# Kernel tuning notes

Measured on AMD Instinct MI355X. Metric: run time of the kernel, lower is better.

Reference implementation:

```python
import jax, jax.numpy as jnp
import numpy as np

HEADS = 8
DIM_HEAD = 128
H = 32
W = 32
SCALE = DIM_HEAD ** (-0.5)


def rel_to_abs(x):
    # x: (b, nh, l, 2l-1) -> (b, nh, l, l) via pad/reshape trick
    b, nh, l, _ = x.shape
    x = jnp.pad(x, ((0, 0), (0, 0), (0, 0), (0, 1)))            # (b,nh,l,2l)
    flat = x.reshape(b, nh, l * 2 * l)
    flat = jnp.pad(flat, ((0, 0), (0, 0), (0, l - 1)))
    final = flat.reshape(b, nh, l + 1, 2 * l - 1)
    return final[:, :, :l, l - 1:]


def relative_logits_1d(q, rel_k):
    # q: (b,n,h,w,d), rel_k: (2w-1,d) -> (b,n,h,h,w,w)
    b, n, h, w, d = q.shape
    logits = jnp.einsum('bnhwd,rd->bnhwr', q, rel_k)
    logits = logits.reshape(b, n * h, w, 2 * w - 1)
    logits = rel_to_abs(logits).reshape(b, n, h, w, w)
    return jnp.broadcast_to(logits[:, :, :, None], (b, n, h, h, w, w))


def rel_pos_logits(q, rel_height, rel_width):
    # q: (b,n,h*w,d) -> (b,n,h*w,h*w)
    b, n, _, d = q.shape
    qh = q.reshape(b, n, H, W, d)
    # width logits: 'b n h H w W -> b n (h w) (H W)'
    rw = relative_logits_1d(qh, rel_width)                       # (b,n,h,H,w,W)
    rw = jnp.transpose(rw, (0, 1, 2, 4, 3, 5)).reshape(b, n, H * W, H * W)
    # height logits: q transposed to (b,n,w,h,d); result 'b n w W h H'
    qt = jnp.transpose(qh, (0, 1, 3, 2, 4))
    rh = relative_logits_1d(qt, rel_height)                      # (b,n,w,W,h,H)
    rh = jnp.transpose(rh, (0, 1, 4, 2, 5, 3)).reshape(b, n, H * W, H * W)
    return rw + rh


def setup_inputs() -> dict:
    key = jax.random.key(0)
    k1, k2, k3, k4 = jax.random.split(key, 4)
    featuremap = jax.random.normal(k1, (8, 512, H, W), dtype=jnp.float32)
    w_qkv = jax.random.normal(k2, (3 * HEADS * DIM_HEAD, 512), dtype=jnp.float32) * 0.02
    rel_height = jax.random.normal(k3, (2 * H - 1, DIM_HEAD), dtype=jnp.float32) * SCALE
    rel_width = jax.random.normal(k4, (2 * W - 1, DIM_HEAD), dtype=jnp.float32) * SCALE
    return {"featuremap": featuremap, "w_qkv": w_qkv,
            "rel_height": rel_height, "rel_width": rel_width}


def reference(featuremap, w_qkv, rel_height, rel_width):
    b, c, h, w = featuremap.shape
    n, d = HEADS, DIM_HEAD
    qkv = jnp.einsum('oc,bchw->bohw', w_qkv, featuremap)         # 1x1 conv, no bias
    q, k, v = jnp.split(qkv, 3, axis=1)

    def to_heads(t):  # 'b (n d) h w -> b n (h w) d'
        return jnp.transpose(t.reshape(b, n, d, h * w), (0, 1, 3, 2))

    q, k, v = to_heads(q), to_heads(k), to_heads(v)
    q = q * SCALE
    logits = jnp.einsum('bnxd,bnyd->bnxy', q, k)
    logits = logits + rel_pos_logits(q, rel_height, rel_width)
    weights = jax.nn.softmax(logits, axis=-1)
    attn_out = jnp.einsum('bnxy,bnyd->bnxd', weights, v)         # (b,n,hw,d)
    # 'b n (h w) d -> b (n d) h w'
    return jnp.transpose(attn_out, (0, 1, 3, 2)).reshape(b, n * d, h, w)
```

## Files before the change

### kernel.cpp

```cpp
#include <hip/hip_runtime.h>

#define BATCH 8
#define CIN   512
#define NH    8
#define DH    128
#define PP    1024
#define QK_SCALE 0.08838834764831845f

typedef unsigned int  u32;
typedef unsigned short u16;
typedef __attribute__((ext_vector_type(8)))  short short8;
typedef __attribute__((ext_vector_type(16))) float f32x16;
typedef __attribute__((ext_vector_type(4)))  u32 u32x4;

typedef __attribute__((address_space(1))) const u32 GU32;
typedef __attribute__((address_space(3))) u32 LU32;


__device__ inline u32 f2bf(float x) {
    u32 u = __float_as_uint(x);
    return (u + 0x7fffu + ((u >> 16) & 1u)) >> 16;
}
__device__ inline float bf2f(u32 h) { return __uint_as_float(h << 16); }

__device__ inline u32 cvtpk(float a, float b) {
    u32 r; asm("v_cvt_pk_bf16_f32 %0, %1, %2" : "=v"(r) : "v"(a), "v"(b)); return r;
}
__device__ inline void split2(float a, float b, u32& wh, u32& wl) {
    u32 h = cvtpk(a, b);
    float ha = __uint_as_float(h << 16);
    float hb = __uint_as_float(h & 0xffff0000u);
    wl = cvtpk(a - ha, b - hb);
    wh = h;
}

__device__ inline void cvt8(const float* v, float scl, uint4& hv, uint4& lv) {
    u32 h[8], l[8];
#pragma unroll
    for (int j = 0; j < 8; ++j) {
        float x = v[j] * scl;
        u32 hb = f2bf(x);
        float hf = bf2f(hb);
        u32 lb = f2bf(x - hf);
        h[j] = hb; l[j] = lb;
    }
    hv = make_uint4(h[0] | (h[1] << 16), h[2] | (h[3] << 16),
                    h[4] | (h[5] << 16), h[6] | (h[7] << 16));
    lv = make_uint4(l[0] | (l[1] << 16), l[2] | (l[3] << 16),
                    l[4] | (l[5] << 16), l[6] | (l[7] << 16));
}

__global__ __launch_bounds__(256) void wconv(
    const float* __restrict__ w, char* __restrict__ AIMG)
{
    const int gid = blockIdx.x * 256 + threadIdx.x;
    const int o  = gid >> 6;
    const int c0 = (gid & 63) << 3;
    const float scl = (o < 1024) ? QK_SCALE : 1.0f;
    float v[8];
    float4 v0 = *(const float4*)(w + (size_t)o * CIN + c0);
    float4 v1 = *(const float4*)(w + (size_t)o * CIN + c0 + 4);
    v[0]=v0.x; v[1]=v0.y; v[2]=v0.z; v[3]=v0.w;
    v[4]=v1.x; v[5]=v1.y; v[6]=v1.z; v[7]=v1.w;
    uint4 hv, lv; cvt8(v, scl, hv, lv);
    const int otile = o >> 7, row = o & 127, chunk = c0 >> 5, g = (c0 >> 3) & 3;
    char* base = AIMG + (size_t)(otile * 16 + chunk) * 16384
               + row * 64 + ((g ^ (row & 3)) << 4);
    *(uint4*)(base)        = hv;
    *(uint4*)(base + 8192) = lv;
}

__global__ __launch_bounds__(256) void fmconv(
    const float* __restrict__ fm, char* __restrict__ FIMG)
{
    __shared__ float Fs[32][128];
    const int t = threadIdx.x;
    const int chunk = blockIdx.x, ptile = blockIdx.y, b = blockIdx.z;
    const float* src = fm + ((size_t)(b * CIN + chunk * 32)) * PP + ptile * 128;
#pragma unroll
    for (int ii = 0; ii < 4; ++ii) {
        int idx = t + 256 * ii;
        int c = idx >> 5, p4 = idx & 31;
        *(float4*)(&Fs[c][p4 * 4]) = *(const float4*)(src + (size_t)c * PP + p4 * 4);
    }
    __syncthreads();
    const int p = t & 127, gb = (t >> 7) * 2;
#pragma unroll
    for (int gi = 0; gi < 2; ++gi) {
        const int g = gb + gi;
        float v[8];
#pragma unroll
        for (int j = 0; j < 8; ++j) v[j] = Fs[g * 8 + j][p];
        uint4 hv, lv; cvt8(v, 1.0f, hv, lv);
        char* base = FIMG + (size_t)((b * 8 + ptile) * 16 + chunk) * 16384
                   + p * 64 + ((g ^ (p & 3)) << 4);
        *(uint4*)(base)        = hv;
        *(uint4*)(base + 8192) = lv;
    }
}

__global__ __launch_bounds__(256) void relprep(
    const float* __restrict__ relH, const float* __restrict__ relW,
    char* __restrict__ RELIMG)
{
    const int idx = blockIdx.x * 256 + threadIdx.x;
    const int r = idx >> 4, g = idx & 15;
    float v[8];
    if (r < 63) {
        float4 v0 = *(const float4*)(relH + (size_t)r * DH + g * 8);
        float4 v1 = *(const float4*)(relH + (size_t)r * DH + g * 8 + 4);
        v[0]=v0.x; v[1]=v0.y; v[2]=v0.z; v[3]=v0.w;
        v[4]=v1.x; v[5]=v1.y; v[6]=v1.z; v[7]=v1.w;
    } else if (r < 126) {
        float4 v0 = *(const float4*)(relW + (size_t)(r - 63) * DH + g * 8);
        float4 v1 = *(const float4*)(relW + (size_t)(r - 63) * DH + g * 8 + 4);
        v[0]=v0.x; v[1]=v0.y; v[2]=v0.z; v[3]=v0.w;
        v[4]=v1.x; v[5]=v1.y; v[6]=v1.z; v[7]=v1.w;
    } else {
#pragma unroll
        for (int j = 0; j < 8; ++j) v[j] = 0.f;
    }
    uint4 hv, lv; cvt8(v, 1.0f, hv, lv);
    char* base = RELIMG + r * 256 + ((g ^ (r & 15)) << 4);
    *(uint4*)(base)         = hv;
    *(uint4*)(base + 32768) = lv;
}

__global__ __launch_bounds__(256, 2) void qkv_gemm(
    const char* __restrict__ AIMG, const char* __restrict__ FIMG,
    u16* __restrict__ Qhi, u16* __restrict__ Qlo,
    char* __restrict__ KIMG, char* __restrict__ VIMG)
{
    __shared__ char lds[65536];

    const int t = threadIdx.x, lane = t & 63, wid = t >> 6;
    const int l31 = lane & 31, h5 = lane >> 5;
    const int ptile = blockIdx.x, otile = blockIdx.y, b = blockIdx.z;
    const int wr = wid >> 1, wc = wid & 1;

    const char* Achunks = AIMG + (size_t)(otile * 16) * 16384;
    const char* Bchunks = FIMG + (size_t)((b * 8 + ptile) * 16) * 16384;

    const int half = wid & 1;
    const char* srcTile = (wid < 2) ? Achunks : Bchunks;
    char* dstBase0 = lds + ((wid < 2) ? 0 : 16384) + half * 8192;

    auto stageChunk = [&](int chunk, int par) {
        const char* src = srcTile + (size_t)chunk * 16384 + half * 8192 + lane * 16;
        char* dst = dstBase0 + par * 32768;
#pragma unroll
        for (int c = 0; c < 8; ++c)
            __builtin_amdgcn_global_load_lds((GU32*)(src + c * 1024),
                                             (LU32*)(dst + c * 1024), 16, 0, 0);
    };

    f32x16 acc[2][2];
#pragma unroll
    for (int i = 0; i < 2; ++i)
#pragma unroll
        for (int j = 0; j < 2; ++j)
#pragma unroll
            for (int r = 0; r < 16; ++r) acc[i][j][r] = 0.f;

    auto computeChunk = [&](int par) {
        const char* Abuf = lds + par * 32768;
        const char* Bbuf = Abuf + 16384;
#pragma unroll
        for (int ks = 0; ks < 2; ++ks) {
            short8 a_h[2], a_l[2], b_h[2], b_l[2];
#pragma unroll
            for (int ot = 0; ot < 2; ++ot) {
                const int row = wr * 64 + ot * 32 + l31;
                const int off = row * 64 + (((ks * 2 + h5) ^ (row & 3)) << 4);
                a_h[ot] = *(const short8*)(Abuf + off);
                a_l[ot] = *(const short8*)(Abuf + 8192 + off);
            }
#pragma unroll
            for (int pt = 0; pt < 2; ++pt) {
                const int col = wc * 64 + pt * 32 + l31;
                const int off = col * 64 + (((ks * 2 + h5) ^ (col & 3)) << 4);
                b_h[pt] = *(const short8*)(Bbuf + off);
                b_l[pt] = *(const short8*)(Bbuf + 8192 + off);
            }
#pragma unroll
            for (int ot = 0; ot < 2; ++ot)
#pragma unroll
                for (int pt = 0; pt < 2; ++pt) {
                    acc[ot][pt] = __builtin_amdgcn_mfma_f32_32x32x16_bf16(a_h[ot], b_h[pt], acc[ot][pt], 0, 0, 0);
                    acc[ot][pt] = __builtin_amdgcn_mfma_f32_32x32x16_bf16(a_h[ot], b_l[pt], acc[ot][pt], 0, 0, 0);
                    acc[ot][pt] = __builtin_amdgcn_mfma_f32_32x32x16_bf16(a_l[ot], b_h[pt], acc[ot][pt], 0, 0, 0);
                }
        }
    };

    stageChunk(0, 0);
    for (int ch = 0; ch < 15; ++ch) {
        stageChunk(ch + 1, (ch + 1) & 1);
        asm volatile("s_waitcnt vmcnt(8)" ::: "memory");
        __builtin_amdgcn_sched_barrier(0);
        __builtin_amdgcn_s_barrier();
        __builtin_amdgcn_sched_barrier(0);
        computeChunk(ch & 1);
        __builtin_amdgcn_s_barrier();
        __builtin_amdgcn_sched_barrier(0);
    }
    asm volatile("s_waitcnt vmcnt(0)" ::: "memory");
    __builtin_amdgcn_sched_barrier(0);
    __builtin_amdgcn_s_barrier();
    __builtin_amdgcn_sched_barrier(0);
    computeChunk(1);
    __syncthreads();

    float* Cs = (float*)lds;
#pragma unroll
    for (int ot = 0; ot < 2; ++ot)
#pragma unroll
        for (int pt = 0; pt < 2; ++pt)
#pragma unroll
            for (int r = 0; r < 16; ++r) {
                const int o = wr * 64 + ot * 32 + (r & 3) + 8 * (r >> 2) + 4 * h5;
                const int p = wc * 64 + pt * 32 + l31;
                Cs[o * 128 + (p ^ (o & 31))] = acc[ot][pt][r];
            }
    __syncthreads();

    const int tsel = otile >> 3;
    const int n    = otile & 7;
    const int bn   = b * NH + n;

    if (tsel == 0) {
        const int d0 = (t & 15) * 8, prow = t >> 4;
#pragma unroll
        for (int i = 0; i < 8; ++i) {
            const int p = prow + 16 * i;
            float v[8];
#pragma unroll
            for (int j = 0; j < 8; ++j)
                v[j] = Cs[(d0 + j) * 128 + (p ^ ((d0 + j) & 31))];
            uint4 hv, lv; cvt8(v, 1.0f, hv, lv);
            const size_t off = ((size_t)bn * PP + ptile * 128 + p) * DH + d0;
            *(uint4*)(Qhi + off) = hv;
            *(uint4*)(Qlo + off) = lv;
        }
    } else if (tsel == 1) {
        const int d0 = (t & 15) * 8, prow = t >> 4;
#pragma unroll
        for (int i = 0; i < 8; ++i) {
            const int p = prow + 16 * i;
            float v[8];
#pragma unroll
            for (int j = 0; j < 8; ++j)
                v[j] = Cs[(d0 + j) * 128 + (p ^ ((d0 + j) & 31))];
            uint4 hv, lv; cvt8(v, 1.0f, hv, lv);
            const int kt = ptile * 4 + (p >> 5), r32 = p & 31;
            char* base = KIMG + ((size_t)(bn * 32 + kt) << 14)
                       + r32 * 256 + (((d0 >> 3) ^ (r32 & 15)) << 4);
            *(uint4*)(base)        = hv;
            *(uint4*)(base + 8192) = lv;
        }
    } else {
        const int g = t & 3, dbase = t >> 2;
#pragma unroll
        for (int i = 0; i < 2; ++i) {
            const int d = dbase + 64 * i;
#pragma unroll
            for (int ks = 0; ks < 4; ++ks) {
                const int p0 = ks * 32 + g * 8;
                float v[8];
#pragma unroll
                for (int j = 0; j < 8; ++j)
                    v[j] = Cs[d * 128 + ((p0 + j) ^ (d & 31))];
                uint4 hv, lv; cvt8(v, 1.0f, hv, lv);
                char* base = VIMG + ((size_t)(bn * 32 + ptile * 4 + ks) << 14)
                           + d * 64 + ((g ^ (d & 3)) << 4);
                *(uint4*)(base)        = hv;
                *(uint4*)(base + 8192) = lv;
            }
        }
    }
}

__global__ __launch_bounds__(256, 1) void rel_gemm(
    const u16* __restrict__ Qhi, const u16* __restrict__ Qlo,
    const char* __restrict__ RELIMG, float* __restrict__ R)
{
    __shared__ char lds[131072];
    const int t = threadIdx.x, lane = t & 63, wid = t >> 6;
    const int l31 = lane & 31, h5 = lane >> 5;
    const int bn = blockIdx.y, p0 = blockIdx.x * 128;

    {
        const char* src = RELIMG + wid * 16384 + lane * 16;
        char* dst = lds + wid * 16384;
#pragma unroll
        for (int c = 0; c < 16; ++c)
            __builtin_amdgcn_global_load_lds((GU32*)(src + c * 1024),
                                             (LU32*)(dst + c * 1024), 16, 0, 0);
    }
#pragma unroll
    for (int pt = 0; pt < 4; ++pt) {
#pragma unroll
        for (int half = 0; half < 2; ++half) {
            const u16* srcp = (half ? Qlo : Qhi) + ((size_t)bn * PP + p0 + pt * 32) * DH;
            char* dstb = lds + 65536 + pt * 16384 + half * 8192;
#pragma unroll
            for (int ii = 0; ii < 2; ++ii) {
                const int f = t + 256 * ii;
                const int p = f >> 4, g = f & 15;
                uint4 v = *(const uint4*)((const char*)srcp + f * 16);
                *(uint4*)(dstb + p * 256 + ((g ^ (p & 15)) << 4)) = v;
            }
        }
    }
    asm volatile("s_waitcnt vmcnt(0) lgkmcnt(0)" ::: "memory");
    __builtin_amdgcn_s_barrier();
    __builtin_amdgcn_sched_barrier(0);

    f32x16 acc[4];
#pragma unroll
    for (int i = 0; i < 4; ++i)
#pragma unroll
        for (int r = 0; r < 16; ++r) acc[i][r] = 0.f;

    const int rrow = wid * 32 + l31;
#pragma unroll
    for (int kk = 0; kk < 8; ++kk) {
        const int g = kk * 2 + h5;
        const int aoff = rrow * 256 + ((g ^ (rrow & 15)) << 4);
        short8 ah = *(const short8*)(lds + aoff);
        short8 al = *(const short8*)(lds + 32768 + aoff);
        const int boff = l31 * 256 + ((g ^ (l31 & 15)) << 4);
#pragma unroll
        for (int pt = 0; pt < 4; ++pt) {
            const char* bb = lds + 65536 + pt * 16384;
            short8 bh = *(const short8*)(bb + boff);
            short8 bl = *(const short8*)(bb + 8192 + boff);
            acc[pt] = __builtin_amdgcn_mfma_f32_32x32x16_bf16(ah, bh, acc[pt], 0, 0, 0);
            acc[pt] = __builtin_amdgcn_mfma_f32_32x32x16_bf16(ah, bl, acc[pt], 0, 0, 0);
            acc[pt] = __builtin_amdgcn_mfma_f32_32x32x16_bf16(al, bh, acc[pt], 0, 0, 0);
        }
    }
    __syncthreads();

    float* Cs = (float*)lds;
#pragma unroll
    for (int pt = 0; pt < 4; ++pt)
#pragma unroll
        for (int r = 0; r < 16; ++r) {
            const int jr = wid * 32 + (r & 3) + 8 * (r >> 2) + 4 * h5;
            Cs[jr * 132 + pt * 32 + l31] = acc[pt][r];
        }
    __syncthreads();

    const int pl = t >> 1, jh = t & 1;
    const int pg = p0 + pl, hq = pg >> 5, wq = pg & 31;
    const int base = jh ? (94 - wq) : (31 - hq);
    float* dst = R + ((size_t)bn * PP + pg) * 64 + jh * 32;
#pragma unroll
    for (int j4 = 0; j4 < 8; ++j4) {
        float4 v;
        v.x = Cs[(base + j4 * 4 + 0) * 132 + pl];
        v.y = Cs[(base + j4 * 4 + 1) * 132 + pl];
        v.z = Cs[(base + j4 * 4 + 2) * 132 + pl];
        v.w = Cs[(base + j4 * 4 + 3) * 132 + pl];
        *(float4*)(dst + j4 * 4) = v;
    }
}

__global__ __launch_bounds__(256, 2) void attn_kernel(
    const u16* __restrict__ Qhi, const u16* __restrict__ Qlo,
    const char* __restrict__ KIMG, const char* __restrict__ VIMG,
    const float* __restrict__ R, float* __restrict__ out)
{
    __shared__ char lds[65536];

    const int t    = threadIdx.x;
    const int lane = t & 63, wid = t >> 6;
    const int lin = blockIdx.x;
    const int bn  = (lin & 7) * 8 + (lin >> 6);
    const int q0  = ((lin >> 3) & 7) * 128;
    const int b  = bn >> 3,  n = bn & 7;
    const int l31 = lane & 31, h5 = lane >> 5;
    const int q_local = wid * 32 + l31;
    const int q = q0 + q_local;

    short8 qh[8], ql[8];
    {
        const u16* qrh = Qhi + ((size_t)bn * PP + q) * DH + h5 * 8;
        const u16* qrl = Qlo + ((size_t)bn * PP + q) * DH + h5 * 8;
#pragma unroll
        for (int kk = 0; kk < 8; ++kk) {
            qh[kk] = *(const short8*)(qrh + kk * 16);
            ql[kk] = *(const short8*)(qrl + kk * 16);
        }
    }
    float R2a[16];
    {
        const float* r2p = R + ((size_t)bn * PP + q) * 64 + 32 + h5 * 4;
#pragma unroll
        for (int m_ = 0; m_ < 4; ++m_) {
            float4 v = *(const float4*)(r2p + m_ * 8);
            R2a[m_*4+0] = v.x; R2a[m_*4+1] = v.y; R2a[m_*4+2] = v.z; R2a[m_*4+3] = v.w;
        }
    }
    float* R1p = (float*)(lds + 49152);
    {
#pragma unroll
        for (int r = 0; r < 4; ++r) {
            int idx = t + 256 * r;
            int row = idx >> 3, c4 = (idx & 7) * 4;
            float4 v = *(const float4*)(R + ((size_t)bn * PP + q0 + row) * 64 + c4);
            R1p[row * 32 + ((c4 + 0) ^ (row & 31))] = v.x;
            R1p[row * 32 + ((c4 + 1) ^ (row & 31))] = v.y;
            R1p[row * 32 + ((c4 + 2) ^ (row & 31))] = v.z;
            R1p[row * 32 + ((c4 + 3) ^ (row & 31))] = v.w;
        }
    }

    auto issueK = [&](int kt, int par) {
        const char* src = KIMG + (((size_t)bn * 32 + kt) << 14) + wid * 4096 + lane * 16;
        const char* dst = lds + par * 16384 + wid * 4096;
#pragma unroll
        for (int c = 0; c < 4; ++c)
            __builtin_amdgcn_global_load_lds((GU32*)(src + c * 1024),
                                             (LU32*)(dst + c * 1024), 16, 0, 0);
    };
    auto issueV = [&](int kt) {
        const char* src = VIMG + (((size_t)bn * 32 + kt) << 14) + wid * 4096 + lane * 16;
        const char* dst = lds + 32768 + wid * 4096;
#pragma unroll
        for (int c = 0; c < 4; ++c)
            __builtin_amdgcn_global_load_lds((GU32*)(src + c * 1024),
                                             (LU32*)(dst + c * 1024), 16, 0, 0);
    };

    issueK(0, 0);
    asm volatile("s_waitcnt lgkmcnt(0)" ::: "memory");
    __builtin_amdgcn_s_barrier();
    __builtin_amdgcn_sched_barrier(0);

    f32x16 o_[4];
#pragma unroll
    for (int i = 0; i < 4; ++i)
#pragma unroll
        for (int r = 0; r < 16; ++r) o_[i][r] = 0.f;

    float m_run = -1e30f, l_run = 0.f;

    for (int kt = 0; kt < 32; ++kt) {
        const int par = kt & 1;
        issueV(kt);
        issueK((kt + 1) & 31, par ^ 1);
        asm volatile("s_waitcnt vmcnt(8)" ::: "memory");
        __builtin_amdgcn_sched_barrier(0);
        __builtin_amdgcn_s_barrier();
        __builtin_amdgcn_sched_barrier(0);

        f32x16 s;
#pragma unroll
        for (int r = 0; r < 16; ++r) s[r] = 0.f;
        const char* kb = lds + par * 16384;
        __builtin_amdgcn_s_setprio(1);
#pragma unroll
        for (int kk = 0; kk < 8; ++kk) {
            const int g = kk * 2 + h5;
            const int off = l31 * 256 + ((g ^ (l31 & 15)) << 4);
            short8 kh = *(const short8*)(kb + off);
            short8 kl = *(const short8*)(kb + 8192 + off);
            s = __builtin_amdgcn_mfma_f32_32x32x16_bf16(kh, qh[kk], s, 0, 0, 0);
            s = __builtin_amdgcn_mfma_f32_32x32x16_bf16(kh, ql[kk], s, 0, 0, 0);
            s = __builtin_amdgcn_mfma_f32_32x32x16_bf16(kl, qh[kk], s, 0, 0, 0);
        }
        __builtin_amdgcn_s_setprio(0);
        const float r1 = R1p[q_local * 32 + (kt ^ l31)];

        float mx = -1e30f;
#pragma unroll
        for (int r = 0; r < 16; ++r) {
            s[r] += R2a[r];
            mx = fmaxf(mx, s[r]);
        }
        mx = fmaxf(mx, __shfl_xor(mx, 32));
        const float pmax = mx + r1;
        if (__any(pmax > m_run + 8.0f)) {
            const float m_new = fmaxf(m_run, pmax);
            const float alpha = __expf(m_run - m_new);
            l_run *= alpha;
#pragma unroll
            for (int i = 0; i < 4; ++i)
#pragma unroll
                for (int r = 0; r < 16; ++r) o_[i][r] *= alpha;
            m_run = m_new;
        }
        const float tsh = r1 - m_run;
        float pf[16];
        float rsum = 0.f;
#pragma unroll
        for (int r = 0; r < 16; ++r) {
            float p = __expf(s[r] + tsh);
            rsum += p;
            pf[r] = p;
        }
        rsum += __shfl_xor(rsum, 32);
        l_run += rsum;

        short8 pH[2], pL[2];
#pragma unroll
        for (int kk2 = 0; kk2 < 2; ++kk2) {
            const int b8 = kk2 * 8;
            u32 h0, l0, h1, l1, h2, l2, h3, l3;
            split2(pf[b8 + 0], pf[b8 + 1], h0, l0);
            split2(pf[b8 + 2], pf[b8 + 3], h1, l1);
            split2(pf[b8 + 4], pf[b8 + 5], h2, l2);
            split2(pf[b8 + 6], pf[b8 + 7], h3, l3);
            asm("v_permlane32_swap_b32 %0, %1" : "+v"(h0), "+v"(h2));
            asm("v_permlane32_swap_b32 %0, %1" : "+v"(h1), "+v"(h3));
            asm("v_permlane32_swap_b32 %0, %1" : "+v"(l0), "+v"(l2));
            asm("v_permlane32_swap_b32 %0, %1" : "+v"(l1), "+v"(l3));
            u32x4 vh = {h0, h1, h2, h3};
            u32x4 vl = {l0, l1, l2, l3};
            pH[kk2] = __builtin_bit_cast(short8, vh);
            pL[kk2] = __builtin_bit_cast(short8, vl);
        }

        asm volatile("s_waitcnt vmcnt(4)" ::: "memory");
        __builtin_amdgcn_sched_barrier(0);
        __builtin_amdgcn_s_barrier();
        __builtin_amdgcn_sched_barrier(0);

        const char* vb = lds + 32768;
        __builtin_amdgcn_s_setprio(1);
#pragma unroll
        for (int kk2 = 0; kk2 < 2; ++kk2) {
#pragma unroll
            for (int nt = 0; nt < 4; ++nt) {
                const int d = nt * 32 + l31;
                const int g = kk2 * 2 + h5;
                const int off = d * 64 + ((g ^ (d & 3)) << 4);
                short8 vh = *(const short8*)(vb + off);
                short8 vl = *(const short8*)(vb + 8192 + off);
                o_[nt] = __builtin_amdgcn_mfma_f32_32x32x16_bf16(vh, pH[kk2], o_[nt], 0, 0, 0);
                o_[nt] = __builtin_amdgcn_mfma_f32_32x32x16_bf16(vl, pH[kk2], o_[nt], 0, 0, 0);
                o_[nt] = __builtin_amdgcn_mfma_f32_32x32x16_bf16(vh, pL[kk2], o_[nt], 0, 0, 0);
            }
        }
        __builtin_amdgcn_s_setprio(0);
        __builtin_amdgcn_s_barrier();
        __builtin_amdgcn_sched_barrier(0);
    }
    asm volatile("s_waitcnt vmcnt(0)" ::: "memory");

    const float inv = 1.f / l_run;
#pragma unroll
    for (int nt = 0; nt < 4; ++nt)
#pragma unroll
        for (int r = 0; r < 16; ++r) {
            const int d = nt * 32 + (r & 3) + ((r >> 2) << 3) + h5 * 4;
            out[((size_t)b * 1024 + n * 128 + d) * PP + q] = o_[nt][r] * inv;
        }
}

extern "C" void kernel_launch(void* const* d_in, const int* in_sizes, int n_in,
                              void* d_out, int out_size, void* d_ws, size_t ws_size,
                              hipStream_t stream)
{
    const float* fm   = (const float*)d_in[0];
    const float* wqkv = (const float*)d_in[1];
    const float* relH = (const float*)d_in[2];
    const float* relW = (const float*)d_in[3];
    float* out = (float*)d_out;

    char* ws = (char*)d_ws;
    u16*  Qhi   = (u16*)(ws);
    u16*  Qlo   = (u16*)(ws + (16ull << 20));
    char* KIMG  = ws + (32ull << 20);
    char* VIMG  = ws + (64ull << 20);
    float* R    = (float*)(ws + (96ull << 20));
    char* FIMG  = ws + (96ull << 20);
    char* AIMG  = ws + (112ull << 20);
    char* RELIMG= ws + (119ull << 20);

    wconv  <<<768, 256, 0, stream>>>(wqkv, AIMG);
    fmconv <<<dim3(16, 8, 8), 256, 0, stream>>>(fm, FIMG);
    relprep<<<8, 256, 0, stream>>>(relH, relW, RELIMG);
    qkv_gemm<<<dim3(8, 24, 8), 256, 0, stream>>>(AIMG, FIMG, Qhi, Qlo, KIMG, VIMG);
    rel_gemm<<<dim3(8, 64), 256, 0, stream>>>(Qhi, Qlo, RELIMG, R);
    attn_kernel<<<512, 256, 0, stream>>>(Qhi, Qlo, KIMG, VIMG, R, out);
}
```

Measured before the change: 283.8 us.

## Software-pipeline QK^T of next tile with softmax/PV and double-buffer V

The attention loop is restructured so the QK^T MFMAs for tile kt+1 are issued before the softmax and PV of tile kt. Two score accumulators alternate, and the loop is unrolled by two. V gets its own double buffer in LDS, growing shared memory to 80KB, which removes the mid-iteration wait and barrier before PV. The log2(e) factor is folded into the Q/K weight scale so exp2f replaces __expf. The aim is more overlap of MFMA work with softmax VALU work and memory waits, at the cost of extra registers and LDS that may threaten two-blocks-per-CU occupancy.

```diff
diff --git a/kernel.cpp b/kernel.cpp
--- a/kernel.cpp
+++ b/kernel.cpp
@@ -6,6 +6,7 @@
 #define DH    128
 #define PP    1024
 #define QK_SCALE 0.08838834764831845f
+#define LOG2E 1.4426950408889634f
 
 typedef unsigned int  u32;
 typedef unsigned short u16;
@@ -56,7 +57,7 @@
     const int gid = blockIdx.x * 256 + threadIdx.x;
     const int o  = gid >> 6;
     const int c0 = (gid & 63) << 3;
-    const float scl = (o < 1024) ? QK_SCALE : 1.0f;
+    const float scl = (o < 1024) ? QK_SCALE * LOG2E : 1.0f;
     float v[8];
     float4 v0 = *(const float4*)(w + (size_t)o * CIN + c0);
     float4 v1 = *(const float4*)(w + (size_t)o * CIN + c0 + 4);
@@ -372,7 +373,7 @@
     const char* __restrict__ KIMG, const char* __restrict__ VIMG,
     const float* __restrict__ R, float* __restrict__ out)
 {
-    __shared__ char lds[65536];
+    __shared__ char lds[81920];
 
     const int t    = threadIdx.x;
     const int lane = t & 63, wid = t >> 6;
@@ -403,7 +404,7 @@
             R2a[m_*4+0] = v.x; R2a[m_*4+1] = v.y; R2a[m_*4+2] = v.z; R2a[m_*4+3] = v.w;
         }
     }
-    float* R1p = (float*)(lds + 49152);
+    float* R1p = (float*)(lds + 65536);
     {
 #pragma unroll
         for (int r = 0; r < 4; ++r) {
@@ -425,9 +426,9 @@
             __builtin_amdgcn_global_load_lds((GU32*)(src + c * 1024),
                                              (LU32*)(dst + c * 1024), 16, 0, 0);
     };
-    auto issueV = [&](int kt) {
+    auto issueV = [&](int kt, int par) {
         const char* src = VIMG + (((size_t)bn * 32 + kt) << 14) + wid * 4096 + lane * 16;
-        const char* dst = lds + 32768 + wid * 4096;
+        const char* dst = lds + 32768 + par * 16384 + wid * 4096;
 #pragma unroll
         for (int c = 0; c < 4; ++c)
             __builtin_amdgcn_global_load_lds((GU32*)(src + c * 1024),
@@ -438,6 +439,12 @@
     asm volatile("s_waitcnt lgkmcnt(0)" ::: "memory");
     __builtin_amdgcn_s_barrier();
     __builtin_amdgcn_sched_barrier(0);
+    issueV(0, 0);
+    issueK(1, 1);
+    asm volatile("s_waitcnt vmcnt(8)" ::: "memory");
+    __builtin_amdgcn_sched_barrier(0);
+    __builtin_amdgcn_s_barrier();
+    __builtin_amdgcn_sched_barrier(0);
 
     f32x16 o_[4];
 #pragma unroll
@@ -446,20 +453,12 @@
         for (int r = 0; r < 16; ++r) o_[i][r] = 0.f;
 
     float m_run = -1e30f, l_run = 0.f;
-
-    for (int kt = 0; kt < 32; ++kt) {
-        const int par = kt & 1;
-        issueV(kt);
-        issueK((kt + 1) & 31, par ^ 1);
-        asm volatile("s_waitcnt vmcnt(8)" ::: "memory");
-        __builtin_amdgcn_sched_barrier(0);
-        __builtin_amdgcn_s_barrier();
-        __builtin_amdgcn_sched_barrier(0);
-
-        f32x16 s;
-#pragma unroll
-        for (int r = 0; r < 16; ++r) s[r] = 0.f;
-        const char* kb = lds + par * 16384;
+    f32x16 sA, sB;
+
+#pragma unroll
+    for (int r = 0; r < 16; ++r) sA[r] = 0.f;
+    {
+        const char* kb = lds;
         __builtin_amdgcn_s_setprio(1);
 #pragma unroll
         for (int kk = 0; kk < 8; ++kk) {
@@ -467,87 +466,120 @@
             const int off = l31 * 256 + ((g ^ (l31 & 15)) << 4);
             short8 kh = *(const short8*)(kb + off);
             short8 kl = *(const short8*)(kb + 8192 + off);
-            s = __builtin_amdgcn_mfma_f32_32x32x16_bf16(kh, qh[kk], s, 0, 0, 0);
-            s = __builtin_amdgcn_mfma_f32_32x32x16_bf16(kh, ql[kk], s, 0, 0, 0);
-            s = __builtin_amdgcn_mfma_f32_32x32x16_bf16(kl, qh[kk], s, 0, 0, 0);
+            sA = __builtin_amdgcn_mfma_f32_32x32x16_bf16(kh, qh[kk], sA, 0, 0, 0);
+            sA = __builtin_amdgcn_mfma_f32_32x32x16_bf16(kh, ql[kk], sA, 0, 0, 0);
+            sA = __builtin_amdgcn_mfma_f32_32x32x16_bf16(kl, qh[kk], sA, 0, 0, 0);
         }
         __builtin_amdgcn_s_setprio(0);
-        const float r1 = R1p[q_local * 32 + (kt ^ l31)];
-
-        float mx = -1e30f;
-#pragma unroll
-        for (int r = 0; r < 16; ++r) {
-            s[r] += R2a[r];
-            mx = fmaxf(mx, s[r]);
-        }
-        mx = fmaxf(mx, __shfl_xor(mx, 32));
-        const float pmax = mx + r1;
-        if (__any(pmax > m_run + 8.0f)) {
-            const float m_new = fmaxf(m_run, pmax);
-            const float alpha = __expf(m_run - m_new);
-            l_run *= alpha;
-#pragma unroll
-            for (int i = 0; i < 4; ++i)
-#pragma unroll
-                for (int r = 0; r < 16; ++r) o_[i][r] *= alpha;
-            m_run = m_new;
-        }
-        const float tsh = r1 - m_run;
-        float pf[16];
-        float rsum = 0.f;
-#pragma unroll
-        for (int r = 0; r < 16; ++r) {
-            float p = __expf(s[r] + tsh);
-            rsum += p;
-            pf[r] = p;
-        }
-        rsum += __shfl_xor(rsum, 32);
-        l_run += rsum;
-
-        short8 pH[2], pL[2];
-#pragma unroll
-        for (int kk2 = 0; kk2 < 2; ++kk2) {
-            const int b8 = kk2 * 8;
-            u32 h0, l0, h1, l1, h2, l2, h3, l3;
-            split2(pf[b8 + 0], pf[b8 + 1], h0, l0);
-            split2(pf[b8 + 2], pf[b8 + 3], h1, l1);
-            split2(pf[b8 + 4], pf[b8 + 5], h2, l2);
-            split2(pf[b8 + 6], pf[b8 + 7], h3, l3);
-            asm("v_permlane32_swap_b32 %0, %1" : "+v"(h0), "+v"(h2));
-            asm("v_permlane32_swap_b32 %0, %1" : "+v"(h1), "+v"(h3));
-            asm("v_permlane32_swap_b32 %0, %1" : "+v"(l0), "+v"(l2));
-            asm("v_permlane32_swap_b32 %0, %1" : "+v"(l1), "+v"(l3));
-            u32x4 vh = {h0, h1, h2, h3};
-            u32x4 vl = {l0, l1, l2, l3};
-            pH[kk2] = __builtin_bit_cast(short8, vh);
-            pL[kk2] = __builtin_bit_cast(short8, vl);
-        }
-
-        asm volatile("s_waitcnt vmcnt(4)" ::: "memory");
-        __builtin_amdgcn_sched_barrier(0);
-        __builtin_amdgcn_s_barrier();
-        __builtin_amdgcn_sched_barrier(0);
-
-        const char* vb = lds + 32768;
-        __builtin_amdgcn_s_setprio(1);
-#pragma unroll
-        for (int kk2 = 0; kk2 < 2; ++kk2) {
-#pragma unroll
-            for (int nt = 0; nt < 4; ++nt) {
-                const int d = nt * 32 + l31;
-                const int g = kk2 * 2 + h5;
-                const int off = d * 64 + ((g ^ (d & 3)) << 4);
-                short8 vh = *(const short8*)(vb + off);
-                short8 vl = *(const short8*)(vb + 8192 + off);
-                o_[nt] = __builtin_amdgcn_mfma_f32_32x32x16_bf16(vh, pH[kk2], o_[nt], 0, 0, 0);
-                o_[nt] = __builtin_amdgcn_mfma_f32_32x32x16_bf16(vl, pH[kk2], o_[nt], 0, 0, 0);
-                o_[nt] = __builtin_amdgcn_mfma_f32_32x32x16_bf16(vh, pL[kk2], o_[nt], 0, 0, 0);
-            }
-        }
-        __builtin_amdgcn_s_setprio(0);
-        __builtin_amdgcn_s_barrier();
-        __builtin_amdgcn_sched_barrier(0);
-    }
+    }
+    __builtin_amdgcn_s_barrier();
+    __builtin_amdgcn_sched_barrier(0);
+
+#define ATTN_ITER(T, SCUR, SNEXT, PAR)                                          \
+    {                                                                           \
+        issueV(((T) + 1) & 31, (PAR) ^ 1);                                      \
+        issueK(((T) + 2) & 31, (PAR));                                          \
+        asm volatile("s_waitcnt vmcnt(8)" ::: "memory");    \
+        __builtin_amdgcn_sched_barrier(0);                                      \
+        __builtin_amdgcn_s_barrier();                                           \
+        __builtin_amdgcn_sched_barrier(0);                                      \
+              \
+        _Pragma("unroll")                                                       \
+        for (int r = 0; r < 16; ++r) SNEXT[r] = 0.f;                            \
+        {                                                                       \
+            const char* kb = lds + ((PAR) ^ 1) * 16384;                         \
+            __builtin_amdgcn_s_setprio(1);                                      \
+            _Pragma("unroll")                                                   \
+            for (int kk = 0; kk < 8; ++kk) {                                    \
+                const int g = kk * 2 + h5;                                      \
+                const int off = l31 * 256 + ((g ^ (l31 & 15)) << 4);            \
+                short8 kh = *(const short8*)(kb + off);                         \
+                short8 kl = *(const short8*)(kb + 8192 + off);                  \
+                SNEXT = __builtin_amdgcn_mfma_f32_32x32x16_bf16(kh, qh[kk], SNEXT, 0, 0, 0); \
+                SNEXT = __builtin_amdgcn_mfma_f32_32x32x16_bf16(kh, ql[kk], SNEXT, 0, 0, 0); \
+                SNEXT = __builtin_amdgcn_mfma_f32_32x32x16_bf16(kl, qh[kk], SNEXT, 0, 0, 0); \
+            }                                                                   \
+            __builtin_amdgcn_s_setprio(0);                                      \
+        }                                                                       \
+                                          \
+        const float r1 = R1p[q_local * 32 + ((T) ^ l31)];                       \
+        float mx = -1e30f;                                                      \
+        _Pragma("unroll")                                                       \
+        for (int r = 0; r < 16; ++r) {                                          \
+            SCUR[r] += R2a[r];                                                  \
+            mx = fmaxf(mx, SCUR[r]);                                            \
+        }                                                                       \
+        mx = fmaxf(mx, __shfl_xor(mx, 32));                                     \
+        const float pmax = mx + r1;                                             \
+        if (__any(pmax > m_run + 11.5415603f)) {                   \
+            const float m_new = fmaxf(m_run, pmax);                             \
+            const float alpha = exp2f(m_run - m_new);                           \
+            l_run *= alpha;                                                     \
+            _Pragma("unroll")                                                   \
+            for (int i = 0; i < 4; ++i)                                         \
+                _Pragma("unroll")                                               \
+                for (int r = 0; r < 16; ++r) o_[i][r] *= alpha;                 \
+            m_run = m_new;                                                      \
+        }                                                                       \
+        const float tsh = r1 - m_run;                                           \
+        float pf[16];                                                           \
+        float rsum = 0.f;                                                       \
+        _Pragma("unroll")                                                       \
+        for (int r = 0; r < 16; ++r) {                                          \
+            float p = exp2f(SCUR[r] + tsh);                                     \
+            rsum += p;                                                          \
+            pf[r] = p;                                                          \
+        }                                                                       \
+        rsum += __shfl_xor(rsum, 32);                                           \
+        l_run += rsum;                                                          \
+        short8 pH[2], pL[2];                                                    \
+        _Pragma("unroll")                                                       \
+        for (int kk2 = 0; kk2 < 2; ++kk2) {                                     \
+            const int b8 = kk2 * 8;                                             \
+            u32 h0, l0, h1, l1, h2, l2, h3, l3;                                 \
+            split2(pf[b8 + 0], pf[b8 + 1], h0, l0);                             \
+            split2(pf[b8 + 2], pf[b8 + 3], h1, l1);                             \
+            split2(pf[b8 + 4], pf[b8 + 5], h2, l2);                             \
+            split2(pf[b8 + 6], pf[b8 + 7], h3, l3);                             \
+            asm("v_permlane32_swap_b32 %0, %1" : "+v"(h0), "+v"(h2));           \
+            asm("v_permlane32_swap_b32 %0, %1" : "+v"(h1), "+v"(h3));           \
+            asm("v_permlane32_swap_b32 %0, %1" : "+v"(l0), "+v"(l2));           \
+            asm("v_permlane32_swap_b32 %0, %1" : "+v"(l1), "+v"(l3));           \
+            u32x4 vh4 = {h0, h1, h2, h3};                                       \
+            u32x4 vl4 = {l0, l1, l2, l3};                                       \
+            pH[kk2] = __builtin_bit_cast(short8, vh4);                          \
+            pL[kk2] = __builtin_bit_cast(short8, vl4);                          \
+        }                                                                       \
+                                                          \
+        {                                                                       \
+            const char* vb = lds + 32768 + (PAR) * 16384;                       \
+            __builtin_amdgcn_s_setprio(1);                                      \
+            _Pragma("unroll")                                                   \
+            for (int kk2 = 0; kk2 < 2; ++kk2) {                                 \
+                _Pragma("unroll")                                               \
+                for (int nt = 0; nt < 4; ++nt) {                                \
+                    const int d = nt * 32 + l31;                                \
+                    const int g = kk2 * 2 + h5;                                 \
+                    const int off = d * 64 + ((g ^ (d & 3)) << 4);              \
+                    short8 vh = *(const short8*)(vb + off);                     \
+                    short8 vl = *(const short8*)(vb + 8192 + off);              \
+                    o_[nt] = __builtin_amdgcn_mfma_f32_32x32x16_bf16(vh, pH[kk2], o_[nt], 0, 0, 0); \
+                    o_[nt] = __builtin_amdgcn_mfma_f32_32x32x16_bf16(vl, pH[kk2], o_[nt], 0, 0, 0); \
+                    o_[nt] = __builtin_amdgcn_mfma_f32_32x32x16_bf16(vh, pL[kk2], o_[nt], 0, 0, 0); \
+                }                                                               \
+            }                                                                   \
+            __builtin_amdgcn_s_setprio(0);                                      \
+        }                                                                       \
+        __builtin_amdgcn_s_barrier();     \
+        __builtin_amdgcn_sched_barrier(0);                                      \
+    }
+
+    for (int tt = 0; tt < 32; tt += 2) {
+        ATTN_ITER(tt,     sA, sB, 0)
+        ATTN_ITER(tt + 1, sB, sA, 1)
+    }
+#undef ATTN_ITER
+
     asm volatile("s_waitcnt vmcnt(0)" ::: "memory");
 
     const float inv = 1.f / l_run;
```

After: 295.4 us. 1.04x slower.
